# Kernel optimization log

Measured on AMD Instinct MI355X. Metric: run time of the kernel, lower is better.

Reference implementation:

```python
import jax, jax.numpy as jnp
import numpy as np

HEADS = 16
DIM_HEAD = 64
SCALE = DIM_HEAD ** -0.5
LN_EPS = 1e-5


def setup_inputs() -> dict:
    key = jax.random.key(0)
    k1, k2, k3 = jax.random.split(key, 3)
    b, s, d = 2, 2048, 1024
    inner = HEADS * DIM_HEAD
    x = jax.random.normal(k1, (b, s, d), dtype=jnp.float32)
    w_qkv = jax.random.normal(k2, (d, 3 * inner), dtype=jnp.float32) * (d ** -0.5)
    w_out = jax.random.normal(k3, (inner, d), dtype=jnp.float32) * (inner ** -0.5)
    return {
        "x": x,
        "ln_gamma": jnp.ones((d,), jnp.float32),
        "ln_beta": jnp.zeros((d,), jnp.float32),
        "w_qkv": w_qkv,
        "w_out": w_out,
        "b_out": jnp.zeros((d,), jnp.float32),
    }


def _layernorm(x, gamma, beta):
    mu = jnp.mean(x, axis=-1, keepdims=True)
    var = jnp.var(x, axis=-1, keepdims=True)
    return (x - mu) * jax.lax.rsqrt(var + LN_EPS) * gamma + beta


def reference(x, ln_gamma, ln_beta, w_qkv, w_out, b_out):
    b, s, d = x.shape
    xn = _layernorm(x, ln_gamma, ln_beta)
    qkv = xn @ w_qkv                       # [b, s, 3*inner]
    q, k, v = jnp.split(qkv, 3, axis=-1)
    def heads(t):
        return t.reshape(b, s, HEADS, DIM_HEAD).transpose(0, 2, 1, 3)  # [b, h, s, dh]
    q, k, v = heads(q), heads(k), heads(v)
    dots = jnp.einsum("bhqd,bhkd->bhqk", q, k) * SCALE   # [b, h, s, s]
    attn = jax.nn.softmax(dots, axis=-1)
    out = jnp.einsum("bhqk,bhkd->bhqd", attn, v)          # [b, h, s, dh]
    out = out.transpose(0, 2, 1, 3).reshape(b, s, HEADS * DIM_HEAD)
    return out @ w_out + b_out
```

## Files before the change

### kernel.cpp

```cpp
#include <hip/hip_runtime.h>
#include <hip/hip_bf16.h>
#include <stdint.h>

#define NH     16
#define DHEAD  64
#define SEQ    2048
#define DMODEL 1024
#define NBATCH 2
#define INNER  1024
#define QKVN   3072
#define ROWS   4096
#define ATT_SCALE 0.125f
#define ATT_QB 64
#define ATT_KB 64

typedef __attribute__((ext_vector_type(8))) __bf16 bf16x8;
typedef __attribute__((ext_vector_type(4))) float floatx4;

__device__ __forceinline__ float bf2f(unsigned short u) {
    union { unsigned int i; float f; } c; c.i = ((unsigned int)u) << 16; return c.f;
}
__device__ __forceinline__ unsigned short f2bf(float f) {
    union { __bf16 b; unsigned short u; } c; c.b = (__bf16)f; return c.u;
}
__device__ __forceinline__ unsigned int pk2(float a, float b) {
    return (unsigned int)f2bf(a) | ((unsigned int)f2bf(b) << 16);
}
__device__ __forceinline__ void storeC(float* p, float v) { *p = v; }
__device__ __forceinline__ void storeC(unsigned short* p, float v) { *p = f2bf(v); }

typedef __attribute__((address_space(1))) void gvoid;
typedef __attribute__((address_space(3))) void lvoid;
__device__ __forceinline__ void gl_lds16(const void* g, void* l) {
    __builtin_amdgcn_global_load_lds((gvoid*)g, (lvoid*)l, 16, 0, 0);
}

__global__ __launch_bounds__(256) void transpose_f2b(
        const float* __restrict__ in, unsigned short* __restrict__ out,
        int rows, int cols) {
    __shared__ unsigned short tile[32][33];
    const int bx = blockIdx.x * 32, by = blockIdx.y * 32;
    const int tx = threadIdx.x & 31, ty = threadIdx.x >> 5;
    for (int i = ty; i < 32; i += 8)
        tile[i][tx] = f2bf(in[(size_t)(by + i) * cols + bx + tx]);
    __syncthreads();
    for (int i = ty; i < 32; i += 8)
        out[(size_t)(bx + i) * rows + by + tx] = tile[tx][i];
}

__global__ __launch_bounds__(256) void ln_kernel(
        const float* __restrict__ x,
        const float* __restrict__ gamma,
        const float* __restrict__ beta,
        unsigned short* __restrict__ xn) {
    __shared__ float red[4][2];
    const int row = blockIdx.x, t = threadIdx.x;
    const size_t base = (size_t)row * DMODEL + t * 4;
    float4 v = *(const float4*)(x + base);
    float s  = v.x + v.y + v.z + v.w;
    float ss = v.x*v.x + v.y*v.y + v.z*v.z + v.w*v.w;
    for (int off = 32; off >= 1; off >>= 1) {
        s  += __shfl_xor(s,  off);
        ss += __shfl_xor(ss, off);
    }
    const int w = t >> 6, lane = t & 63;
    if (lane == 0) { red[w][0] = s; red[w][1] = ss; }
    __syncthreads();
    if (t == 0) {
        float S  = red[0][0] + red[1][0] + red[2][0] + red[3][0];
        float SS = red[0][1] + red[1][1] + red[2][1] + red[3][1];
        float mu  = S * (1.f / DMODEL);
        float var = SS * (1.f / DMODEL) - mu * mu;
        red[0][0] = mu; red[0][1] = rsqrtf(var + 1e-5f);
    }
    __syncthreads();
    const float mu = red[0][0], rstd = red[0][1];
    float4 g = *(const float4*)(gamma + t * 4);
    float4 bb = *(const float4*)(beta + t * 4);
    ushort4 o;
    o.x = f2bf((v.x - mu) * rstd * g.x + bb.x);
    o.y = f2bf((v.y - mu) * rstd * g.y + bb.y);
    o.z = f2bf((v.z - mu) * rstd * g.z + bb.z);
    o.w = f2bf((v.w - mu) * rstd * g.w + bb.w);
    *(ushort4*)(xn + base) = o;
}

__global__ __launch_bounds__(256) void gemm_qkv(
        const unsigned short* __restrict__ A,
        const unsigned short* __restrict__ Bt,
        unsigned short* __restrict__ qP,
        unsigned short* __restrict__ kP,
        unsigned short* __restrict__ vT) {
    const int K = DMODEL;
    __shared__ __align__(16) unsigned short sA[128 * 32];
    __shared__ __align__(16) unsigned short sB[128 * 32];
    const int t = threadIdx.x;
    const int mBase = blockIdx.y * 128, nBase = blockIdx.x * 128;
    const int w = t >> 6, lane = t & 63, quad = lane >> 4, l16 = lane & 15;
    const int wm = (w >> 1) * 64, wn = (w & 1) * 64;
    const int srow = t >> 2, sch = t & 3;
    floatx4 acc[4][4];
    for (int mi = 0; mi < 4; mi++)
        for (int ni = 0; ni < 4; ni++) acc[mi][ni] = (floatx4)0.f;

    for (int k0 = 0; k0 < K; k0 += 32) {
        #pragma unroll
        for (int c = 0; c < 2; c++) {
            const int row = c * 64 + srow;
            const int gcol = (sch ^ ((row >> 1) & 3)) * 8;
            gl_lds16(&A[(size_t)(mBase + row) * K + k0 + gcol], &sA[(c * 256 + w * 64) * 8]);
            gl_lds16(&Bt[(size_t)(nBase + row) * K + k0 + gcol], &sB[(c * 256 + w * 64) * 8]);
        }
        __syncthreads();
        bf16x8 af[4], bfv[4];
        #pragma unroll
        for (int mi = 0; mi < 4; mi++) {
            const int r = wm + mi * 16 + l16;
            af[mi] = *(const bf16x8*)&sA[r * 32 + (quad ^ ((r >> 1) & 3)) * 8];
        }
        #pragma unroll
        for (int ni = 0; ni < 4; ni++) {
            const int r = wn + ni * 16 + l16;
            bfv[ni] = *(const bf16x8*)&sB[r * 32 + (quad ^ ((r >> 1) & 3)) * 8];
        }
        #pragma unroll
        for (int mi = 0; mi < 4; mi++)
            #pragma unroll
            for (int ni = 0; ni < 4; ni++)
                acc[mi][ni] = __builtin_amdgcn_mfma_f32_16x16x32_bf16(
                    af[mi], bfv[ni], acc[mi][ni], 0, 0, 0);
        __syncthreads();
    }
    #pragma unroll
    for (int ni = 0; ni < 4; ni++) {
        const int col = nBase + wn + ni * 16 + l16;
        const int reg = col >> 10;
        const int h   = (col & 1023) >> 6;
        const int dh  = col & 63;
        #pragma unroll
        for (int mi = 0; mi < 4; mi++) {
            const int row0 = mBase + wm + mi * 16 + quad * 4;
            const int b = row0 >> 11, s0 = row0 & 2047;
            const int bh = b * NH + h;
            if (reg == 2) {
                ushort4 o;
                o.x = f2bf(acc[mi][ni][0]); o.y = f2bf(acc[mi][ni][1]);
                o.z = f2bf(acc[mi][ni][2]); o.w = f2bf(acc[mi][ni][3]);
                *(ushort4*)&vT[((size_t)bh * DHEAD + dh) * SEQ + s0] = o;
            } else {
                unsigned short* dst = (reg == 0 ? qP : kP);
                #pragma unroll
                for (int i = 0; i < 4; i++)
                    dst[((size_t)bh * SEQ + s0 + i) * DHEAD + dh] = f2bf(acc[mi][ni][i]);
            }
        }
    }
}

__global__ __launch_bounds__(256) void gemm_out(
        const unsigned short* __restrict__ A,
        const unsigned short* __restrict__ Bt,
        float* __restrict__ C,
        const int M, const int N, const int K,
        const float* __restrict__ bias) {
    __shared__ __align__(16) unsigned short sA[128 * 32];
    __shared__ __align__(16) unsigned short sB[128 * 32];
    const int t = threadIdx.x;
    const int mBase = blockIdx.y * 128, nBase = blockIdx.x * 128;
    const int w = t >> 6, lane = t & 63, quad = lane >> 4, l16 = lane & 15;
    const int wm = (w >> 1) * 64, wn = (w & 1) * 64;
    const int srow = t >> 2, sch = t & 3;
    floatx4 acc[4][4];
    for (int mi = 0; mi < 4; mi++)
        for (int ni = 0; ni < 4; ni++) acc[mi][ni] = (floatx4)0.f;

    for (int k0 = 0; k0 < K; k0 += 32) {
        #pragma unroll
        for (int c = 0; c < 2; c++) {
            const int row = c * 64 + srow;
            const int gcol = (sch ^ ((row >> 1) & 3)) * 8;
            gl_lds16(&A[(size_t)(mBase + row) * K + k0 + gcol], &sA[(c * 256 + w * 64) * 8]);
            gl_lds16(&Bt[(size_t)(nBase + row) * K + k0 + gcol], &sB[(c * 256 + w * 64) * 8]);
        }
        __syncthreads();
        bf16x8 af[4], bfv[4];
        #pragma unroll
        for (int mi = 0; mi < 4; mi++) {
            const int r = wm + mi * 16 + l16;
            af[mi] = *(const bf16x8*)&sA[r * 32 + (quad ^ ((r >> 1) & 3)) * 8];
        }
        #pragma unroll
        for (int ni = 0; ni < 4; ni++) {
            const int r = wn + ni * 16 + l16;
            bfv[ni] = *(const bf16x8*)&sB[r * 32 + (quad ^ ((r >> 1) & 3)) * 8];
        }
        #pragma unroll
        for (int mi = 0; mi < 4; mi++)
            #pragma unroll
            for (int ni = 0; ni < 4; ni++)
                acc[mi][ni] = __builtin_amdgcn_mfma_f32_16x16x32_bf16(
                    af[mi], bfv[ni], acc[mi][ni], 0, 0, 0);
        __syncthreads();
    }
    #pragma unroll
    for (int mi = 0; mi < 4; mi++)
        #pragma unroll
        for (int ni = 0; ni < 4; ni++) {
            const int col = nBase + wn + ni * 16 + l16;
            const float badd = bias ? bias[col] : 0.f;
            #pragma unroll
            for (int i = 0; i < 4; i++) {
                const int row = mBase + wm + mi * 16 + quad * 4 + i;
                C[(size_t)row * N + col] = acc[mi][ni][i] + badd;
            }
        }
}

__global__ __launch_bounds__(256, 4) void attn_kernel(
        const unsigned short* __restrict__ qP,
        const unsigned short* __restrict__ kP,
        const unsigned short* __restrict__ vT,
        unsigned short* __restrict__ aout) {
    __shared__ __align__(16) unsigned short sK[2][ATT_KB * 64];
    __shared__ __align__(16) unsigned short sV[2][ATT_KB * 64];
    const int t = threadIdx.x, w = t >> 6, lane = t & 63;
    const int quad = lane >> 4, l16 = lane & 15;
    const int bh = blockIdx.y;
    const int qrow = blockIdx.x * ATT_QB + w * 16 + l16;
    const int swr = l16 & 7;

    const unsigned short* qb = qP + ((size_t)bh * SEQ + qrow) * DHEAD;
    bf16x8 aq[2];
    aq[0] = *(const bf16x8*)(qb + quad * 8);
    aq[1] = *(const bf16x8*)(qb + 32 + quad * 8);

    floatx4 oac[4];
    float mS = -1e30f, lS = 0.f;
    #pragma unroll
    for (int c = 0; c < 4; c++) oac[c] = (floatx4)0.f;

    const unsigned short* kb = kP + (size_t)bh * SEQ * DHEAD;
    const unsigned short* vb = vT + (size_t)bh * DHEAD * SEQ;
    const int r8 = lane >> 3, sw8 = ((lane & 7) ^ r8) * 8;

    auto stage = [&](int it, int bi) {
        const int kv0 = it * ATT_KB;
        #pragma unroll
        for (int ii = 0; ii < 2; ii++) {
            const int row = w * 16 + ii * 8 + r8;
            gl_lds16(kb + (size_t)(kv0 + row) * DHEAD + sw8,
                     (void*)&sK[bi][(w * 16 + ii * 8) * 64]);
            gl_lds16(vb + (size_t)row * SEQ + kv0 + sw8,
                     (void*)&sV[bi][(w * 16 + ii * 8) * 64]);
        }
    };
    stage(0, 0);

    const int adrA = ((quad & 1) * 32 + l16) * 4;
    const int adrB = adrA + 64;

    for (int it = 0; it < SEQ / ATT_KB; ++it) {
        __syncthreads();
        if (it + 1 < SEQ / ATT_KB) stage(it + 1, (it + 1) & 1);
        const unsigned short* sKb = &sK[it & 1][0];
        const unsigned short* sVb = &sV[it & 1][0];

        bf16x8 kf[4][2];
        #pragma unroll
        for (int c = 0; c < 4; c++)
            #pragma unroll
            for (int hh = 0; hh < 2; hh++)
                kf[c][hh] = *(const bf16x8*)&sKb[(c * 16 + l16) * 64 +
                                                 8 * (((hh << 2) | quad) ^ swr)];
        floatx4 sv[4];
        #pragma unroll
        for (int c = 0; c < 4; c++) {
            floatx4 a = (floatx4)0.f;
            a = __builtin_amdgcn_mfma_f32_16x16x32_bf16(kf[c][0], aq[0], a, 0, 0, 0);
            a = __builtin_amdgcn_mfma_f32_16x16x32_bf16(kf[c][1], aq[1], a, 0, 0, 0);
            sv[c] = a;
        }
        float mx = -1e30f;
        #pragma unroll
        for (int c = 0; c < 4; c++)
            #pragma unroll
            for (int i = 0; i < 4; i++) {
                sv[c][i] *= ATT_SCALE;
                mx = fmaxf(mx, sv[c][i]);
            }
        mx = fmaxf(mx, __shfl_xor(mx, 16));
        mx = fmaxf(mx, __shfl_xor(mx, 32));
        const float nm = fmaxf(mS, mx);
        const float al = __expf(mS - nm);
        mS = nm;
        float sum = 0.f;
        uint2 pkc[4];
        #pragma unroll
        for (int c = 0; c < 4; c++) {
            float p0 = __expf(sv[c][0] - nm), p1 = __expf(sv[c][1] - nm);
            float p2 = __expf(sv[c][2] - nm), p3 = __expf(sv[c][3] - nm);
            sum += (p0 + p1) + (p2 + p3);
            pkc[c].x = pk2(p0, p1);
            pkc[c].y = pk2(p2, p3);
        }
        sum += __shfl_xor(sum, 16);
        sum += __shfl_xor(sum, 32);
        lS = lS * al + sum;
        #pragma unroll
        for (int c = 0; c < 4; c++) oac[c] *= al;

        const bool sel = (quad < 2);
        bf16x8 pf[2];
        #pragma unroll
        for (int hh = 0; hh < 2; hh++) {
            const uint2 cl = pkc[2 * hh], ch = pkc[2 * hh + 1];
            int a0 = __builtin_amdgcn_ds_bpermute(adrA, (int)cl.x);
            int b0 = __builtin_amdgcn_ds_bpermute(adrA, (int)ch.x);
            int a1 = __builtin_amdgcn_ds_bpermute(adrA, (int)cl.y);
            int b1 = __builtin_amdgcn_ds_bpermute(adrA, (int)ch.y);
            int a2 = __builtin_amdgcn_ds_bpermute(adrB, (int)cl.x);
            int b2 = __builtin_amdgcn_ds_bpermute(adrB, (int)ch.x);
            int a3 = __builtin_amdgcn_ds_bpermute(adrB, (int)cl.y);
            int b3 = __builtin_amdgcn_ds_bpermute(adrB, (int)ch.y);
            union { int i[4]; bf16x8 v; } u;
            u.i[0] = sel ? a0 : b0;
            u.i[1] = sel ? a1 : b1;
            u.i[2] = sel ? a2 : b2;
            u.i[3] = sel ? a3 : b3;
            pf[hh] = u.v;
        }
        #pragma unroll
        for (int c = 0; c < 4; c++) {
            bf16x8 v0 = *(const bf16x8*)&sVb[(c * 16 + l16) * 64 + 8 * ((quad) ^ swr)];
            bf16x8 v1 = *(const bf16x8*)&sVb[(c * 16 + l16) * 64 + 8 * ((4 | quad) ^ swr)];
            oac[c] = __builtin_amdgcn_mfma_f32_16x16x32_bf16(v0, pf[0], oac[c], 0, 0, 0);
            oac[c] = __builtin_amdgcn_mfma_f32_16x16x32_bf16(v1, pf[1], oac[c], 0, 0, 0);
        }
    }
    const float rl = 1.f / lS;
    const int b = bh >> 4, h = bh & 15;
    const size_t rowb = ((size_t)(b * SEQ + qrow)) * INNER + h * DHEAD;
    #pragma unroll
    for (int c = 0; c < 4; c++) {
        ushort4 o;
        o.x = f2bf(oac[c][0] * rl);
        o.y = f2bf(oac[c][1] * rl);
        o.z = f2bf(oac[c][2] * rl);
        o.w = f2bf(oac[c][3] * rl);
        *(ushort4*)&aout[rowb + c * 16 + quad * 4] = o;
    }
}

extern "C" void kernel_launch(void* const* d_in, const int* in_sizes, int n_in,
                              void* d_out, int out_size, void* d_ws, size_t ws_size,
                              hipStream_t stream) {
    const float* x     = (const float*)d_in[0];
    const float* gamma = (const float*)d_in[1];
    const float* beta  = (const float*)d_in[2];
    const float* wqkv  = (const float*)d_in[3];
    const float* wout  = (const float*)d_in[4];
    const float* bout  = (const float*)d_in[5];
    float* out = (float*)d_out;

    unsigned short* ws     = (unsigned short*)d_ws;
    unsigned short* xn     = ws;
    unsigned short* wqkvT  = xn     + (size_t)ROWS * DMODEL;
    unsigned short* qPb    = wqkvT  + (size_t)QKVN * DMODEL;
    unsigned short* kPb    = qPb    + (size_t)NBATCH * NH * SEQ * DHEAD;
    unsigned short* vTb    = kPb    + (size_t)NBATCH * NH * SEQ * DHEAD;
    unsigned short* attnO  = vTb    + (size_t)NBATCH * NH * SEQ * DHEAD;
    unsigned short* woutT  = attnO  + (size_t)ROWS * INNER;

    transpose_f2b<<<dim3(QKVN / 32, DMODEL / 32), 256, 0, stream>>>(wqkv, wqkvT, DMODEL, QKVN);
    transpose_f2b<<<dim3(DMODEL / 32, INNER / 32), 256, 0, stream>>>(wout, woutT, INNER, DMODEL);
    ln_kernel<<<ROWS, 256, 0, stream>>>(x, gamma, beta, xn);
    gemm_qkv<<<dim3(QKVN / 128, ROWS / 128), 256, 0, stream>>>(xn, wqkvT, qPb, kPb, vTb);
    attn_kernel<<<dim3(SEQ / ATT_QB, NBATCH * NH), 256, 0, stream>>>(qPb, kPb, vTb, attnO);
    gemm_out<<<dim3(DMODEL / 128, ROWS / 128), 256, 0, stream>>>(
        attnO, woutT, out, ROWS, DMODEL, INNER, bout);
}
```

Measured before the change: 233.0 us.

## Process four query tiles per wave in attention and stage Q/K epilogue through LDS

The attention kernel now runs 128 threads, each wave owning 64 query rows (four 16-row tiles). K and V fragments are loaded from LDS once per KV block and reused across all four tiles. The probability transpose now goes through a per-wave LDS scratch buffer instead of ds_bpermute shuffles. The QKV GEMM epilogue for Q and K writes through an LDS tile so each lane stores full 64-element rows with 16-byte writes instead of scattered 2-byte stores. In exchange, per-thread register use and LDS traffic per tile go up, and the attention grid has half as many blocks.

```diff
diff --git a/kernel.cpp b/kernel.cpp
--- a/kernel.cpp
+++ b/kernel.cpp
@@ -11,7 +11,7 @@
 #define QKVN   3072
 #define ROWS   4096
 #define ATT_SCALE 0.125f
-#define ATT_QB 64
+#define ATT_QB 128
 #define ATT_KB 64
 
 typedef __attribute__((ext_vector_type(8))) __bf16 bf16x8;
@@ -23,11 +23,6 @@
 __device__ __forceinline__ unsigned short f2bf(float f) {
     union { __bf16 b; unsigned short u; } c; c.b = (__bf16)f; return c.u;
 }
-__device__ __forceinline__ unsigned int pk2(float a, float b) {
-    return (unsigned int)f2bf(a) | ((unsigned int)f2bf(b) << 16);
-}
-__device__ __forceinline__ void storeC(float* p, float v) { *p = v; }
-__device__ __forceinline__ void storeC(unsigned short* p, float v) { *p = f2bf(v); }
 
 typedef __attribute__((address_space(1))) void gvoid;
 typedef __attribute__((address_space(3))) void lvoid;
@@ -94,6 +89,7 @@
     const int K = DMODEL;
     __shared__ __align__(16) unsigned short sA[128 * 32];
     __shared__ __align__(16) unsigned short sB[128 * 32];
+    __shared__ __align__(16) unsigned short tb[2][64 * 72];
     const int t = threadIdx.x;
     const int mBase = blockIdx.y * 128, nBase = blockIdx.x * 128;
     const int w = t >> 6, lane = t & 63, quad = lane >> 4, l16 = lane & 15;
@@ -131,28 +127,46 @@
                     af[mi], bfv[ni], acc[mi][ni], 0, 0, 0);
         __syncthreads();
     }
-    #pragma unroll
-    for (int ni = 0; ni < 4; ni++) {
-        const int col = nBase + wn + ni * 16 + l16;
-        const int reg = col >> 10;
-        const int h   = (col & 1023) >> 6;
-        const int dh  = col & 63;
-        #pragma unroll
-        for (int mi = 0; mi < 4; mi++) {
-            const int row0 = mBase + wm + mi * 16 + quad * 4;
-            const int b = row0 >> 11, s0 = row0 & 2047;
-            const int bh = b * NH + h;
-            if (reg == 2) {
+    const int reg = nBase >> 10;
+    if (reg == 2) {
+        #pragma unroll
+        for (int ni = 0; ni < 4; ni++) {
+            const int col = nBase + wn + ni * 16 + l16;
+            const int h = (col & 1023) >> 6, dh = col & 63;
+            #pragma unroll
+            for (int mi = 0; mi < 4; mi++) {
+                const int row0 = mBase + wm + mi * 16 + quad * 4;
+                const int b = row0 >> 11, s0 = row0 & 2047;
                 ushort4 o;
                 o.x = f2bf(acc[mi][ni][0]); o.y = f2bf(acc[mi][ni][1]);
                 o.z = f2bf(acc[mi][ni][2]); o.w = f2bf(acc[mi][ni][3]);
-                *(ushort4*)&vT[((size_t)bh * DHEAD + dh) * SEQ + s0] = o;
-            } else {
-                unsigned short* dst = (reg == 0 ? qP : kP);
+                *(ushort4*)&vT[((size_t)(b * NH + h) * DHEAD + dh) * SEQ + s0] = o;
+            }
+        }
+    } else {
+        unsigned short* dst = (reg == 0) ? qP : kP;
+        const int hh = ((nBase + wn) & 1023) >> 6;
+        #pragma unroll
+        for (int ph = 0; ph < 2; ph++) {
+            if ((w >> 1) == ph) {
+                unsigned short* tb_ = &tb[w & 1][0];
                 #pragma unroll
-                for (int i = 0; i < 4; i++)
-                    dst[((size_t)bh * SEQ + s0 + i) * DHEAD + dh] = f2bf(acc[mi][ni][i]);
-            }
+                for (int mi = 0; mi < 4; mi++)
+                    #pragma unroll
+                    for (int ni = 0; ni < 4; ni++)
+                        #pragma unroll
+                        for (int i = 0; i < 4; i++)
+                            tb_[(mi * 16 + quad * 4 + i) * 72 + ni * 16 + l16] =
+                                f2bf(acc[mi][ni][i]);
+                asm volatile("s_waitcnt lgkmcnt(0)" ::: "memory");
+                const int row_g = mBase + wm + lane;
+                const int b = row_g >> 11, sr = row_g & 2047;
+                unsigned short* orow = dst + ((size_t)(b * NH + hh) * SEQ + sr) * DHEAD;
+                #pragma unroll
+                for (int c = 0; c < 8; c++)
+                    *(bf16x8*)&orow[c * 8] = *(const bf16x8*)&tb_[lane * 72 + c * 8];
+            }
+            __syncthreads();
         }
     }
 }
@@ -216,28 +230,36 @@
         }
 }
 
-__global__ __launch_bounds__(256, 4) void attn_kernel(
+__global__ __launch_bounds__(128) void attn_kernel(
         const unsigned short* __restrict__ qP,
         const unsigned short* __restrict__ kP,
         const unsigned short* __restrict__ vT,
         unsigned short* __restrict__ aout) {
     __shared__ __align__(16) unsigned short sK[2][ATT_KB * 64];
     __shared__ __align__(16) unsigned short sV[2][ATT_KB * 64];
+    __shared__ __align__(16) unsigned short sP[2][16 * 72];
     const int t = threadIdx.x, w = t >> 6, lane = t & 63;
     const int quad = lane >> 4, l16 = lane & 15;
-    const int bh = blockIdx.y;
-    const int qrow = blockIdx.x * ATT_QB + w * 16 + l16;
-    const int swr = l16 & 7;
-
-    const unsigned short* qb = qP + ((size_t)bh * SEQ + qrow) * DHEAD;
-    bf16x8 aq[2];
-    aq[0] = *(const bf16x8*)(qb + quad * 8);
-    aq[1] = *(const bf16x8*)(qb + 32 + quad * 8);
-
-    floatx4 oac[4];
-    float mS = -1e30f, lS = 0.f;
+    const int bh = blockIdx.y, b = bh >> 4, h = bh & 15;
+    const int qb0 = blockIdx.x * ATT_QB + w * 64;
+    const int sx = l16 & 7;
+
+    bf16x8 aq[4][2];
     #pragma unroll
-    for (int c = 0; c < 4; c++) oac[c] = (floatx4)0.f;
+    for (int qt = 0; qt < 4; qt++)
+        #pragma unroll
+        for (int kc = 0; kc < 2; kc++)
+            aq[qt][kc] = *(const bf16x8*)&qP[
+                ((size_t)bh * SEQ + qb0 + qt * 16 + l16) * DHEAD + kc * 32 + quad * 8];
+
+    floatx4 oac[4][4];
+    float mS[4], lS[4];
+    #pragma unroll
+    for (int qt = 0; qt < 4; qt++) {
+        mS[qt] = -1e30f; lS[qt] = 0.f;
+        #pragma unroll
+        for (int d = 0; d < 4; d++) oac[qt][d] = (floatx4)0.f;
+    }
 
     const unsigned short* kb = kP + (size_t)bh * SEQ * DHEAD;
     const unsigned short* vb = vT + (size_t)bh * DHEAD * SEQ;
@@ -246,18 +268,15 @@
     auto stage = [&](int it, int bi) {
         const int kv0 = it * ATT_KB;
         #pragma unroll
-        for (int ii = 0; ii < 2; ii++) {
-            const int row = w * 16 + ii * 8 + r8;
+        for (int ii = 0; ii < 4; ii++) {
+            const int row = w * 32 + ii * 8 + r8;
             gl_lds16(kb + (size_t)(kv0 + row) * DHEAD + sw8,
-                     (void*)&sK[bi][(w * 16 + ii * 8) * 64]);
+                     (void*)&sK[bi][(w * 32 + ii * 8) * 64]);
             gl_lds16(vb + (size_t)row * SEQ + kv0 + sw8,
-                     (void*)&sV[bi][(w * 16 + ii * 8) * 64]);
+                     (void*)&sV[bi][(w * 32 + ii * 8) * 64]);
         }
     };
     stage(0, 0);
-
-    const int adrA = ((quad & 1) * 32 + l16) * 4;
-    const int adrB = adrA + 64;
 
     for (int it = 0; it < SEQ / ATT_KB; ++it) {
         __syncthreads();
@@ -265,89 +284,77 @@
         const unsigned short* sKb = &sK[it & 1][0];
         const unsigned short* sVb = &sV[it & 1][0];
 
-        bf16x8 kf[4][2];
-        #pragma unroll
-        for (int c = 0; c < 4; c++)
-            #pragma unroll
-            for (int hh = 0; hh < 2; hh++)
-                kf[c][hh] = *(const bf16x8*)&sKb[(c * 16 + l16) * 64 +
-                                                 8 * (((hh << 2) | quad) ^ swr)];
-        floatx4 sv[4];
-        #pragma unroll
-        for (int c = 0; c < 4; c++) {
-            floatx4 a = (floatx4)0.f;
-            a = __builtin_amdgcn_mfma_f32_16x16x32_bf16(kf[c][0], aq[0], a, 0, 0, 0);
-            a = __builtin_amdgcn_mfma_f32_16x16x32_bf16(kf[c][1], aq[1], a, 0, 0, 0);
-            sv[c] = a;
-        }
-        float mx = -1e30f;
-        #pragma unroll
-        for (int c = 0; c < 4; c++)
-            #pragma unroll
-            for (int i = 0; i < 4; i++) {
-                sv[c][i] *= ATT_SCALE;
-                mx = fmaxf(mx, sv[c][i]);
-            }
-        mx = fmaxf(mx, __shfl_xor(mx, 16));
-        mx = fmaxf(mx, __shfl_xor(mx, 32));
-        const float nm = fmaxf(mS, mx);
-        const float al = __expf(mS - nm);
-        mS = nm;
-        float sum = 0.f;
-        uint2 pkc[4];
-        #pragma unroll
-        for (int c = 0; c < 4; c++) {
-            float p0 = __expf(sv[c][0] - nm), p1 = __expf(sv[c][1] - nm);
-            float p2 = __expf(sv[c][2] - nm), p3 = __expf(sv[c][3] - nm);
-            sum += (p0 + p1) + (p2 + p3);
-            pkc[c].x = pk2(p0, p1);
-            pkc[c].y = pk2(p2, p3);
-        }
-        sum += __shfl_xor(sum, 16);
-        sum += __shfl_xor(sum, 32);
-        lS = lS * al + sum;
-        #pragma unroll
-        for (int c = 0; c < 4; c++) oac[c] *= al;
-
-        const bool sel = (quad < 2);
-        bf16x8 pf[2];
-        #pragma unroll
-        for (int hh = 0; hh < 2; hh++) {
-            const uint2 cl = pkc[2 * hh], ch = pkc[2 * hh + 1];
-            int a0 = __builtin_amdgcn_ds_bpermute(adrA, (int)cl.x);
-            int b0 = __builtin_amdgcn_ds_bpermute(adrA, (int)ch.x);
-            int a1 = __builtin_amdgcn_ds_bpermute(adrA, (int)cl.y);
-            int b1 = __builtin_amdgcn_ds_bpermute(adrA, (int)ch.y);
-            int a2 = __builtin_amdgcn_ds_bpermute(adrB, (int)cl.x);
-            int b2 = __builtin_amdgcn_ds_bpermute(adrB, (int)ch.x);
-            int a3 = __builtin_amdgcn_ds_bpermute(adrB, (int)cl.y);
-            int b3 = __builtin_amdgcn_ds_bpermute(adrB, (int)ch.y);
-            union { int i[4]; bf16x8 v; } u;
-            u.i[0] = sel ? a0 : b0;
-            u.i[1] = sel ? a1 : b1;
-            u.i[2] = sel ? a2 : b2;
-            u.i[3] = sel ? a3 : b3;
-            pf[hh] = u.v;
-        }
-        #pragma unroll
-        for (int c = 0; c < 4; c++) {
-            bf16x8 v0 = *(const bf16x8*)&sVb[(c * 16 + l16) * 64 + 8 * ((quad) ^ swr)];
-            bf16x8 v1 = *(const bf16x8*)&sVb[(c * 16 + l16) * 64 + 8 * ((4 | quad) ^ swr)];
-            oac[c] = __builtin_amdgcn_mfma_f32_16x16x32_bf16(v0, pf[0], oac[c], 0, 0, 0);
-            oac[c] = __builtin_amdgcn_mfma_f32_16x16x32_bf16(v1, pf[1], oac[c], 0, 0, 0);
-        }
-    }
-    const float rl = 1.f / lS;
-    const int b = bh >> 4, h = bh & 15;
-    const size_t rowb = ((size_t)(b * SEQ + qrow)) * INNER + h * DHEAD;
+        bf16x8 kf[4][2], vf[4][2];
+        #pragma unroll
+        for (int r = 0; r < 4; r++)
+            #pragma unroll
+            for (int kc = 0; kc < 2; kc++) {
+                const int cp = ((kc * 4 + quad) ^ sx) * 8;
+                kf[r][kc] = *(const bf16x8*)&sKb[(r * 16 + l16) * 64 + cp];
+                vf[r][kc] = *(const bf16x8*)&sVb[(r * 16 + l16) * 64 + cp];
+            }
+        unsigned short* pw = &sP[w][0];
+        #pragma unroll
+        for (int qt = 0; qt < 4; qt++) {
+            floatx4 sv[4];
+            #pragma unroll
+            for (int kvt = 0; kvt < 4; kvt++) {
+                floatx4 a = (floatx4)0.f;
+                a = __builtin_amdgcn_mfma_f32_16x16x32_bf16(kf[kvt][0], aq[qt][0], a, 0, 0, 0);
+                a = __builtin_amdgcn_mfma_f32_16x16x32_bf16(kf[kvt][1], aq[qt][1], a, 0, 0, 0);
+                sv[kvt] = a;
+            }
+            float mx = -1e30f;
+            #pragma unroll
+            for (int kvt = 0; kvt < 4; kvt++)
+                #pragma unroll
+                for (int i = 0; i < 4; i++) {
+                    sv[kvt][i] *= ATT_SCALE;
+                    mx = fmaxf(mx, sv[kvt][i]);
+                }
+            mx = fmaxf(mx, __shfl_xor(mx, 16));
+            mx = fmaxf(mx, __shfl_xor(mx, 32));
+            const float nm = fmaxf(mS[qt], mx);
+            const float al = __expf(mS[qt] - nm);
+            mS[qt] = nm;
+            float sum = 0.f;
+            #pragma unroll
+            for (int kvt = 0; kvt < 4; kvt++) {
+                float p0 = __expf(sv[kvt][0] - nm), p1 = __expf(sv[kvt][1] - nm);
+                float p2 = __expf(sv[kvt][2] - nm), p3 = __expf(sv[kvt][3] - nm);
+                sum += (p0 + p1) + (p2 + p3);
+                ushort4 pk;
+                pk.x = f2bf(p0); pk.y = f2bf(p1); pk.z = f2bf(p2); pk.w = f2bf(p3);
+                *(ushort4*)&pw[l16 * 72 + kvt * 16 + quad * 4] = pk;
+            }
+            sum += __shfl_xor(sum, 16);
+            sum += __shfl_xor(sum, 32);
+            lS[qt] = lS[qt] * al + sum;
+            #pragma unroll
+            for (int d = 0; d < 4; d++) oac[qt][d] *= al;
+            asm volatile("s_waitcnt lgkmcnt(0)" ::: "memory");
+            const bf16x8 pf0 = *(const bf16x8*)&pw[l16 * 72 + quad * 8];
+            const bf16x8 pf1 = *(const bf16x8*)&pw[l16 * 72 + 32 + quad * 8];
+            #pragma unroll
+            for (int d = 0; d < 4; d++) {
+                oac[qt][d] = __builtin_amdgcn_mfma_f32_16x16x32_bf16(vf[d][0], pf0, oac[qt][d], 0, 0, 0);
+                oac[qt][d] = __builtin_amdgcn_mfma_f32_16x16x32_bf16(vf[d][1], pf1, oac[qt][d], 0, 0, 0);
+            }
+        }
+    }
     #pragma unroll
-    for (int c = 0; c < 4; c++) {
-        ushort4 o;
-        o.x = f2bf(oac[c][0] * rl);
-        o.y = f2bf(oac[c][1] * rl);
-        o.z = f2bf(oac[c][2] * rl);
-        o.w = f2bf(oac[c][3] * rl);
-        *(ushort4*)&aout[rowb + c * 16 + quad * 4] = o;
+    for (int qt = 0; qt < 4; qt++) {
+        const float rl = 1.f / lS[qt];
+        const size_t rowb = ((size_t)(b * SEQ + qb0 + qt * 16 + l16)) * INNER + h * DHEAD;
+        #pragma unroll
+        for (int d = 0; d < 4; d++) {
+            ushort4 o;
+            o.x = f2bf(oac[qt][d][0] * rl);
+            o.y = f2bf(oac[qt][d][1] * rl);
+            o.z = f2bf(oac[qt][d][2] * rl);
+            o.w = f2bf(oac[qt][d][3] * rl);
+            *(ushort4*)&aout[rowb + d * 16 + quad * 4] = o;
+        }
     }
 }
 
@@ -375,7 +382,7 @@
     transpose_f2b<<<dim3(DMODEL / 32, INNER / 32), 256, 0, stream>>>(wout, woutT, INNER, DMODEL);
     ln_kernel<<<ROWS, 256, 0, stream>>>(x, gamma, beta, xn);
     gemm_qkv<<<dim3(QKVN / 128, ROWS / 128), 256, 0, stream>>>(xn, wqkvT, qPb, kPb, vTb);
-    attn_kernel<<<dim3(SEQ / ATT_QB, NBATCH * NH), 256, 0, stream>>>(qPb, kPb, vTb, attnO);
+    attn_kernel<<<dim3(SEQ / ATT_QB, NBATCH * NH), 128, 0, stream>>>(qPb, kPb, vTb, attnO);
     gemm_out<<<dim3(DMODEL / 128, ROWS / 128), 256, 0, stream>>>(
         attnO, woutT, out, ROWS, DMODEL, INNER, bout);
 }
```

Result: slower. 245.7 us (+5.5%).
